# Optimization experiments

Measured on AMD Instinct MI355X. Metric: run time of the kernel, lower is better.

Reference implementation:

```python
import jax, jax.numpy as jnp
import numpy as np

V = 10000  # vocab_size
E = 128    # embedding_dim
H = 256    # per-layer hidden size
B = 32     # batch
S = 512    # seq_len


def setup_inputs() -> dict:
    key = jax.random.key(0)
    ks = jax.random.split(key, 8)
    input_x = jax.random.randint(ks[0], (B, S), 0, V, dtype=jnp.int32)
    input_y = jax.random.randint(ks[1], (B, S), 0, V, dtype=jnp.int32)
    input_lengths = jax.random.randint(ks[2], (B,), 1, S + 1, dtype=jnp.int32)
    emb_W = jax.random.uniform(ks[3], (V, E), minval=-1.0, maxval=1.0, dtype=jnp.float32)
    k0 = jax.random.normal(ks[4], (E + H, 4 * H), dtype=jnp.float32) * 0.05
    b0 = jnp.zeros((4 * H,), jnp.float32)
    k1 = jax.random.normal(ks[5], (H + H, 4 * H), dtype=jnp.float32) * 0.05
    b1 = jnp.zeros((4 * H,), jnp.float32)
    out_W = jax.random.normal(ks[6], (H, V), dtype=jnp.float32) * 0.05
    out_b = jnp.zeros((V,), jnp.float32)
    return dict(input_x=input_x, input_y=input_y, input_lengths=input_lengths,
                emb_W=emb_W, k0=k0, b0=b0, k1=k1, b1=b1, out_W=out_W, out_b=out_b)


def _lstm_layer(xs, lengths, kernel, bias):
    """TF LSTMCell semantics: gate order i,g,f,o; forget_bias=1.0.
    xs: [S,B,D] -> ys: [S,B,H]; dynamic_rnn masking: state frozen and
    output zeroed for t >= lengths."""
    Sd, Bd, _ = xs.shape
    Hd = bias.shape[0] // 4
    f1 = jnp.asarray(1.0, xs.dtype)

    def step(carry, inp):
        h, c = carry
        x, t = inp
        z = jnp.concatenate([x, h], axis=-1) @ kernel + bias  # [B,4H]
        i, g, f, o = jnp.split(z, 4, axis=-1)
        c_new = jax.nn.sigmoid(f + f1) * c + jax.nn.sigmoid(i) * jnp.tanh(g)
        h_new = jax.nn.sigmoid(o) * jnp.tanh(c_new)
        active = (t < lengths)[:, None]
        h2 = jnp.where(active, h_new, h)
        c2 = jnp.where(active, c_new, c)
        out = jnp.where(active, h_new, jnp.zeros_like(h_new))
        return (h2, c2), out

    init = (jnp.zeros((Bd, Hd), xs.dtype), jnp.zeros((Bd, Hd), xs.dtype))
    _, ys = jax.lax.scan(step, init, (xs, jnp.arange(Sd)))
    return ys


def reference(input_x, input_y, input_lengths, emb_W, k0, b0, k1, b1, out_W, out_b):
    emb = emb_W[input_x]                 # [B,S,E] embedding lookup
    xs = jnp.swapaxes(emb, 0, 1)         # [S,B,E]
    h1 = _lstm_layer(xs, input_lengths, k0, b0)
    h2 = _lstm_layer(h1, input_lengths, k1, b1)
    outputs = jnp.swapaxes(h2, 0, 1)     # [B,S,H]
    scores = outputs @ out_W + out_b     # [B,S,V]
    logp = jax.nn.log_softmax(scores, axis=-1)
    xent = -jnp.take_along_axis(logp, input_y[..., None], axis=-1)[..., 0]  # [B,S]
    mask = jnp.sign(input_y.astype(scores.dtype))  # label 0 is padding
    per_ex = jnp.sum(mask * xent, axis=1) / input_lengths.astype(scores.dtype)
    return jnp.mean(per_ex)
```

## Files before the change

kernel.cpp:

```cpp
#include <hip/hip_runtime.h>
#include <hip/hip_fp8.h>
#include <cmath>

#define SS 512
#define BB 32
#define EE 128
#define HH 256
#define VV 10000
#define NROWS (SS*BB)
#define VPAD 10048
#define NT8 (VPAD/16)

typedef unsigned short ushort_t;
typedef unsigned char uchar_t;
typedef __attribute__((ext_vector_type(8))) short bf16x8;
typedef __attribute__((ext_vector_type(8))) int i32x8;
typedef __attribute__((ext_vector_type(4))) float f32x4;

#define MFMA(a,b,c)  __builtin_amdgcn_mfma_f32_16x16x32_bf16((a),(b),(c),0,0,0)
#define MFMAS(a,b,c) __builtin_amdgcn_mfma_scale_f32_16x16x128_f8f6f4((a),(b),(c),0,0,0,0x7F7F7F7F,0,0x7F7F7F7F)

__device__ __forceinline__ ushort_t f2bf(float x) {
    unsigned u = __float_as_uint(x);
    u = (u + 0x7FFFu + ((u >> 16) & 1u)) >> 16;
    return (ushort_t)u;
}
__device__ __forceinline__ float bf2f(ushort_t h) {
    return __uint_as_float(((unsigned)h) << 16);
}
__device__ __forceinline__ uchar_t f2fp8(float x) {
    __hip_fp8_e4m3 t(x);
    return (uchar_t)t.__x;
}
__device__ __forceinline__ float sigf(float x) { return 1.0f / (1.0f + __expf(-x)); }
__device__ __forceinline__ float tanhf_(float x) { return 1.0f - 2.0f / (__expf(2.0f * x) + 1.0f); }

__device__ __forceinline__ i32x8 ldfrag(const uchar_t* base, int lane) {
    i32x8 r;
    ((uint4*)&r)[0] = *(const uint4*)(base + lane * 16);
    ((uint4*)&r)[1] = *(const uint4*)(base + 1024 + lane * 16);
    return r;
}

__device__ __forceinline__ void pollc(unsigned* p, unsigned target) {
    int it = 0;
    while (__hip_atomic_load(p, __ATOMIC_RELAXED, __HIP_MEMORY_SCOPE_AGENT) < target) {
        __builtin_amdgcn_s_sleep(4);
        if (++it > 50000000) break;
    }
}
__device__ __forceinline__ void reladd(unsigned* p) {
    __hip_atomic_fetch_add(p, 1u, __ATOMIC_RELEASE, __HIP_MEMORY_SCOPE_AGENT);
}

__global__ __launch_bounds__(256)
void prep_kernel(const float* __restrict__ k0, const float* __restrict__ k1,
                 const float* __restrict__ out_W, const float* __restrict__ out_b,
                 ushort_t* __restrict__ W1xT, uchar_t* __restrict__ Wsw1,
                 uchar_t* __restrict__ Wsw2, ushort_t* __restrict__ W2x,
                 uchar_t* __restrict__ Wt8, float* __restrict__ obp)
{
    __shared__ float tile[64][65];
    const int blk = blockIdx.x;
    const int tid = threadIdx.x;

    if (blk < 32) {
        const int n0 = (blk & 15) * 64, k0_ = (blk >> 4) * 64;
        for (int i = tid; i < 4096; i += 256) {
            const int kk = i >> 6, nn = i & 63;
            tile[kk][nn] = k0[(size_t)(k0_ + kk) * 1024 + n0 + nn];
        }
        __syncthreads();
        for (int i = tid; i < 4096; i += 256) {
            const int nn = i >> 6, kk = i & 63;
            W1xT[(size_t)(n0 + nn) * 128 + k0_ + kk] = f2bf(tile[kk][nn]);
        }
    } else if (blk < 160) {
        const bool l2 = (blk >= 96);
        const int nt = l2 ? (blk - 96) : (blk - 32);
        const float* src = l2 ? (k1 + (size_t)HH * 1024) : (k0 + (size_t)EE * 1024);
        uchar_t* dst = l2 ? Wsw2 : Wsw1;
        const int kk = tid >> 7, h = (tid >> 6) & 1, l = tid & 63;
        const int q = l >> 4, n16 = l & 15;
        const int col = (nt >> 4) * 256 + (nt & 15) * 16 + n16;
        uchar_t v[16];
#pragma unroll
        for (int j = 0; j < 16; j++) {
            const int k = kk * 128 + q * 32 + h * 16 + j;
            v[j] = f2fp8(src[(size_t)k * 1024 + col]);
        }
        *(uint4*)&dst[(((size_t)(nt * 2 + kk) * 2 + h) * 64 + l) * 16] = *(uint4*)v;
    } else if (blk < 224) {
        const int r = blk - 160;
        const int n0 = (r & 15) * 64, k0_ = (r >> 4) * 64;
        for (int i = tid; i < 4096; i += 256) {
            const int kk = i >> 6, nn = i & 63;
            tile[kk][nn] = k1[(size_t)(k0_ + kk) * 1024 + n0 + nn];
        }
        __syncthreads();
        for (int i = tid; i < 4096; i += 256) {
            const int nn = i >> 6, kk = i & 63;
            W2x[(size_t)(n0 + nn) * 256 + k0_ + kk] = f2bf(tile[kk][nn]);
        }
    } else if (blk < 224 + NT8) {
        const int nt = blk - 224;
        const int kk = tid >> 7, h = (tid >> 6) & 1, l = tid & 63;
        const int q = l >> 4, n16 = l & 15;
        const int col = nt * 16 + n16;
        uchar_t v[16];
#pragma unroll
        for (int j = 0; j < 16; j++) {
            const int k = kk * 128 + q * 32 + h * 16 + j;
            v[j] = (col < VV) ? f2fp8(out_W[(size_t)k * VV + col]) : (uchar_t)0;
        }
        *(uint4*)&Wt8[(((size_t)(nt * 2 + kk) * 2 + h) * 64 + l) * 16] = *(uint4*)v;
    } else {
        const int v = (blk - 224 - NT8) * 256 + tid;
        if (v < VPAD) obp[v] = (v < VV) ? out_b[v] : -INFINITY;
    }
}

__global__ __launch_bounds__(256)
void zgemm_mf(const ushort_t* __restrict__ W1xT, const float* __restrict__ b0v,
              const float* __restrict__ emb, const int* __restrict__ idx,
              ushort_t* __restrict__ Zb)
{
    __shared__ ushort_t ash[64 * 136];
    const int tid = threadIdx.x;
    const int w = tid >> 6, lane = tid & 63;
    const int q = lane >> 4, n16 = lane & 15;
    const int m0 = blockIdx.x * 64;
    const int nbase = blockIdx.y * 256;

    for (int i = tid; i < 64 * 32; i += 256) {
        const int r_ = i >> 5, c4 = i & 31;
        const int m = m0 + r_;
        const int t = m >> 5, b = m & 31;
        const int id = idx[b * SS + t];
        const float4 v = ((const float4*)emb)[(size_t)id * 32 + c4];
        ushort_t o4[4] = { f2bf(v.x), f2bf(v.y), f2bf(v.z), f2bf(v.w) };
        *(uint2*)&ash[r_ * 136 + c4 * 4] = *(uint2*)o4;
    }
    __syncthreads();

    bf16x8 A[4];
#pragma unroll
    for (int kb = 0; kb < 4; kb++)
        A[kb] = *(const bf16x8*)&ash[(w * 16 + n16) * 136 + kb * 32 + q * 8];

#pragma unroll 1
    for (int nt = 0; nt < 16; nt++) {
        const int n = nbase + nt * 16 + n16;
        bf16x8 B[4];
#pragma unroll
        for (int kb = 0; kb < 4; kb++)
            B[kb] = *(const bf16x8*)&W1xT[(size_t)n * 128 + kb * 32 + q * 8];
        f32x4 C = (f32x4){0.f, 0.f, 0.f, 0.f};
#pragma unroll
        for (int kb = 0; kb < 4; kb++)
            C = MFMA(A[kb], B[kb], C);
        const float bv = b0v[n];
        const int g = n >> 8, u = n & 255;
#pragma unroll
        for (int r = 0; r < 4; r++)
            Zb[(size_t)(m0 + w * 16 + q * 4 + r) * 1024 + u * 4 + g] = f2bf(C[r] + bv);
    }
}

__device__ __forceinline__ void lstm_role(
    uchar_t* Bl, uchar_t* h8buf,
    const uchar_t* __restrict__ Wsw, const ushort_t* __restrict__ zin,
    const int* __restrict__ lens, ushort_t* __restrict__ outp,
    uchar_t* __restrict__ hf8,
    unsigned* prog1, unsigned* xflag, unsigned* h2prog,
    int b, bool isL1)
{
    uchar_t (*h8)[256] = (uchar_t (*)[256])h8buf;
    const int tid = threadIdx.x;
    const int w = tid >> 6, lane = tid & 63;
    const int q = lane >> 4, n16 = lane & 15;
    const int len = lens[b];
    const int jown = q >> 1;
    const int unit = w * 32 + jown * 16 + n16;

#pragma unroll
    for (int li = 0; li < 3; li++) {
        const int nt = li * 16 + w * 2 + 1;
#pragma unroll
        for (int fh = 0; fh < 4; fh++) {
            const size_t s = (((size_t)nt * 4 + fh) * 64 + lane) * 16;
            const size_t d = (((size_t)(w * 3 + li) * 4 + fh) * 64 + lane) * 16;
            *(uint4*)&Bl[d] = *(const uint4*)&Wsw[s];
        }
    }
    i32x8 Bv[4][2];
#pragma unroll
    for (int g = 0; g < 4; g++) {
        const int nt = g * 16 + w * 2;
#pragma unroll
        for (int kk = 0; kk < 2; kk++)
            Bv[g][kk] = ldfrag(&Wsw[(size_t)nt * 4096 + kk * 2048], lane);
    }
    i32x8 Sv[2];
    {
        const int nt = 3 * 16 + w * 2 + 1;
#pragma unroll
        for (int kk = 0; kk < 2; kk++)
            Sv[kk] = ldfrag(&Wsw[(size_t)nt * 4096 + kk * 2048], lane);
    }
    if (tid < 256) { h8[0][tid] = 0; h8[1][tid] = 0; }
    float c = 0.f;
    __syncthreads();

    const uchar_t* Lb0 = &Bl[(size_t)(w * 3) * 4096];

    uint2 zreg;
    bool zvalid = false;
    if (isL1) {
        zreg = *(const uint2*)&zin[(size_t)(0 * 32 + b) * 1024 + unit * 4];
        zvalid = true;
    }

    for (int t = 0; t < SS; t++) {
        if (t >= len) {
            uint4 zz; zz.x = zz.y = zz.z = zz.w = 0u;
            if (outp) {
                const int nseg = (SS - t) * 32;
                for (int i = tid; i < nseg; i += 512) {
                    const int tt = t + (i >> 5), seg = i & 31;
                    *(uint4*)&outp[((size_t)tt * 32 + b) * 256 + seg * 8] = zz;
                }
            }
            if (hf8) {
                const int nseg8 = (SS - t) * 16;
                for (int i = tid; i < nseg8; i += 512) {
                    const int tt = t + (i >> 4), seg = i & 15;
                    *(uint4*)&hf8[((size_t)tt * 32 + b) * 256 + seg * 16] = zz;
                }
            }
            __syncthreads();
            if (tid == 0) {
                if (isL1) for (int cc = t >> 5; cc < 16; cc++) reladd(&prog1[cc]);
                else      for (int cc = t >> 3; cc < 64; cc++) reladd(&h2prog[cc]);
            }
            break;
        }
        if (!isL1 && (t & 31) == 0) {
            if (tid == 0) {
#pragma unroll
                for (int cc = 0; cc < 4; cc++) pollc(&xflag[(t >> 3) + cc], 1u);
            }
            __syncthreads();
            __builtin_amdgcn_fence(__ATOMIC_ACQUIRE, "agent");
        }
        const size_t row = (size_t)t * 32 + b;
        ushort_t z4[4];
        if (zvalid) *(uint2*)z4 = zreg;
        else        *(uint2*)z4 = *(const uint2*)&zin[row * 1024 + unit * 4];
        if (t + 1 < SS && (isL1 || ((t + 1) & 31) != 0)) {
            zreg = *(const uint2*)&zin[(row + 32) * 1024 + unit * 4];
            zvalid = true;
        } else zvalid = false;

        const int rd = t & 1, wr = rd ^ 1;
        i32x8 Af0, Af1;
        ((uint4*)&Af0)[0] = *(const uint4*)&h8[rd][q * 32];
        ((uint4*)&Af0)[1] = *(const uint4*)&h8[rd][q * 32 + 16];
        ((uint4*)&Af1)[0] = *(const uint4*)&h8[rd][128 + q * 32];
        ((uint4*)&Af1)[1] = *(const uint4*)&h8[rd][128 + q * 32 + 16];

        float gvv[4];
#pragma unroll
        for (int g = 0; g < 4; g++) {
            f32x4 C0 = (f32x4){0.f,0.f,0.f,0.f}, C1 = (f32x4){0.f,0.f,0.f,0.f};
            C0 = MFMAS(Af0, Bv[g][0], C0);
            C0 = MFMAS(Af1, Bv[g][1], C0);
            if (g < 3) {
                const uchar_t* p = Lb0 + (size_t)g * 4096;
                C1 = MFMAS(Af0, ldfrag(p, lane), C1);
                C1 = MFMAS(Af1, ldfrag(p + 2048, lane), C1);
            } else {
                C1 = MFMAS(Af0, Sv[0], C1);
                C1 = MFMAS(Af1, Sv[1], C1);
            }
            gvv[g] = jown ? C1[0] : C0[0];
        }
        {
            const float zi = bf2f(z4[0]) + gvv[0];
            const float zg = bf2f(z4[1]) + gvv[1];
            const float zf = bf2f(z4[2]) + gvv[2];
            const float zo = bf2f(z4[3]) + gvv[3];
            const float cn = sigf(zf + 1.0f) * c + sigf(zi) * tanhf_(zg);
            const float hn = sigf(zo) * tanhf_(cn);
            c = cn;
            const uchar_t h8v = f2fp8(hn);
            h8[wr][unit] = h8v;
            if (outp) outp[row * 256 + unit] = f2bf(hn);
            if (hf8) hf8[row * 256 + unit] = h8v;
        }
        __syncthreads();
        if (tid == 0) {
            if (isL1) { if (((t + 1) & 31) == 0) reladd(&prog1[t >> 5]); }
            else      { if (((t + 1) & 7)  == 0) reladd(&h2prog[t >> 3]); }
        }
    }
}

__global__ __launch_bounds__(512, 1)
void pipe_kernel(const uchar_t* __restrict__ Wsw1, const uchar_t* __restrict__ Wsw2,
                 const ushort_t* __restrict__ W2x, const float* __restrict__ b1v,
                 const int* __restrict__ lens, const ushort_t* __restrict__ Zb,
                 ushort_t* __restrict__ out1, ushort_t* __restrict__ Xp,
                 uchar_t* __restrict__ hf8, const uchar_t* __restrict__ Wt8,
                 const float* __restrict__ obp, const int* __restrict__ y,
                 float* __restrict__ out,
                 unsigned* __restrict__ prog1, unsigned* __restrict__ xflag,
                 unsigned* __restrict__ h2prog)
{
    __shared__ uchar_t smem[98816];
    const int tid = threadIdx.x;
    const int blk = blockIdx.x;
    const int w = tid >> 6, lane = tid & 63;
    const int q = lane >> 4, n16 = lane & 15;

    if (blk < 32) {
        lstm_role(smem, smem + 98304, Wsw1, Zb, lens, out1, nullptr,
                  prog1, xflag, h2prog, blk, true);
    } else if (blk < 96) {
        ushort_t* ash = (ushort_t*)smem;
        const int b2 = blk - 32;
        if (tid == 0) pollc(&prog1[b2 >> 2], 32u);
        __syncthreads();
        __builtin_amdgcn_fence(__ATOMIC_ACQUIRE, "agent");
#pragma unroll 1
        for (int half = 0; half < 2; half++) {
            const int m0 = b2 * 256 + half * 128;
            if (half) __syncthreads();
            for (int i = tid; i < 128 * 32; i += 512) {
                const int r_ = i >> 5, s_ = i & 31;
                *(uint4*)&ash[r_ * 264 + s_ * 8] =
                    *(const uint4*)&out1[(size_t)(m0 + r_) * 256 + s_ * 8];
            }
            __syncthreads();
#pragma unroll 1
            for (int i = 0; i < 8; i++) {
                const int n = (w * 8 + i) * 16 + n16;
                bf16x8 Bfr[8];
#pragma unroll
                for (int kb = 0; kb < 8; kb++)
                    Bfr[kb] = *(const bf16x8*)&W2x[(size_t)n * 256 + kb * 32 + q * 8];
                const float bval = b1v[n];
                const int g = n >> 8, u = n & 255;
                f32x4 Cc[8];
#pragma unroll
                for (int mt = 0; mt < 8; mt++) {
                    Cc[mt] = (f32x4){0.f, 0.f, 0.f, 0.f};
                    bf16x8 Af[8];
#pragma unroll
                    for (int kb = 0; kb < 8; kb++)
                        Af[kb] = *(const bf16x8*)&ash[(mt * 16 + n16) * 264 + kb * 32 + q * 8];
#pragma unroll
                    for (int kb = 0; kb < 8; kb++)
                        Cc[mt] = MFMA(Af[kb], Bfr[kb], Cc[mt]);
                }
#pragma unroll
                for (int mt = 0; mt < 8; mt++)
#pragma unroll
                    for (int r = 0; r < 4; r++) {
                        const int rrow = m0 + mt * 16 + q * 4 + r;
                        Xp[(size_t)rrow * 1024 + u * 4 + g] = f2bf(Cc[mt][r] + bval);
                    }
            }
        }
        __syncthreads();
        if (tid == 0)
            __hip_atomic_store(&xflag[b2], 1u, __ATOMIC_RELEASE, __HIP_MEMORY_SCOPE_AGENT);
    } else if (blk < 128) {
        lstm_role(smem, smem + 98304, Wsw2, Xp, lens, nullptr, hf8,
                  prog1, xflag, h2prog, blk - 96, false);
    } else {
        float* lsw = (float*)smem;
        float* tgt64 = (float*)(smem + 1024);
        const int cb = blk - 128;
        if (tid == 0) pollc(&h2prog[cb >> 1], 32u);
        __syncthreads();
        __builtin_amdgcn_fence(__ATOMIC_ACQUIRE, "agent");
#pragma unroll 1
        for (int half = 0; half < 2; half++) {
            const int m0 = cb * 128 + half * 64;
            __syncthreads();
            if (tid < 64) tgt64[tid] = 0.f;
            i32x8 A8[4][2];
            int yv[16];
            float lsum[16];
            if (tid < 256) {
#pragma unroll
                for (int mt = 0; mt < 4; mt++) {
                    const size_t rbase = (size_t)(m0 + mt * 16 + n16) * 256;
#pragma unroll
                    for (int kk = 0; kk < 2; kk++) {
                        ((uint4*)&A8[mt][kk])[0] = *(const uint4*)&hf8[rbase + kk * 128 + q * 32];
                        ((uint4*)&A8[mt][kk])[1] = *(const uint4*)&hf8[rbase + kk * 128 + q * 32 + 16];
                    }
                }
#pragma unroll
                for (int mt = 0; mt < 4; mt++)
#pragma unroll
                    for (int r = 0; r < 4; r++) {
                        const int m = m0 + mt * 16 + q * 4 + r;
                        yv[mt * 4 + r] = y[(m & 31) * SS + (m >> 5)];
                    }
#pragma unroll
                for (int i = 0; i < 16; i++) lsum[i] = 0.f;
            }
            __syncthreads();
            if (tid < 256) {
                for (int tile = 0; tile < 157; tile++) {
                    const int nt = w * 157 + tile;
                    const int n = nt * 16 + n16;
                    const i32x8 B0 = ldfrag(&Wt8[(size_t)(nt * 2 + 0) * 2048], lane);
                    const i32x8 B1 = ldfrag(&Wt8[(size_t)(nt * 2 + 1) * 2048], lane);
                    const float obv = obp[n];
                    f32x4 C[4];
#pragma unroll
                    for (int mt = 0; mt < 4; mt++) {
                        C[mt] = (f32x4){0.f, 0.f, 0.f, 0.f};
                        C[mt] = MFMAS(A8[mt][0], B0, C[mt]);
                        C[mt] = MFMAS(A8[mt][1], B1, C[mt]);
                    }
#pragma unroll
                    for (int mt = 0; mt < 4; mt++)
#pragma unroll
                        for (int r = 0; r < 4; r++) {
                            const float sc = C[mt][r] + obv;
                            if (n == yv[mt * 4 + r]) tgt64[mt * 16 + q * 4 + r] = sc;
                            lsum[mt * 4 + r] += __expf(sc - 16.0f);
                        }
                }
#pragma unroll
                for (int i = 0; i < 16; i++) {
                    float v = lsum[i];
                    v += __shfl_xor(v, 1, 16); v += __shfl_xor(v, 2, 16);
                    v += __shfl_xor(v, 4, 16); v += __shfl_xor(v, 8, 16);
                    lsum[i] = v;
                }
                if (n16 == 0)
#pragma unroll
                    for (int i = 0; i < 16; i++)
                        lsw[w * 64 + (i >> 2) * 16 + q * 4 + (i & 3)] = lsum[i];
            }
            __syncthreads();
            if (tid < 64) {
                const float l = lsw[tid] + lsw[64 + tid] + lsw[128 + tid] + lsw[192 + tid];
                const float lse = 16.0f + __logf(l);
                const int m = m0 + tid;
                const int tt = m >> 5, bb = m & 31;
                const int yvv = y[bb * SS + tt];
                float local = (yvv != 0) ? (lse - tgt64[tid]) / (32.0f * (float)lens[bb]) : 0.f;
                for (int off = 1; off < 64; off <<= 1) local += __shfl_xor(local, off, 64);
                if (tid == 0) atomicAdd(out, local);
            }
        }
    }
}

extern "C" void kernel_launch(void* const* d_in, const int* in_sizes, int n_in,
                              void* d_out, int out_size, void* d_ws, size_t ws_size,
                              hipStream_t stream)
{
    const int*   input_x = (const int*)  d_in[0];
    const int*   input_y = (const int*)  d_in[1];
    const int*   lens    = (const int*)  d_in[2];
    const float* emb_W   = (const float*)d_in[3];
    const float* k0      = (const float*)d_in[4];
    const float* b0      = (const float*)d_in[5];
    const float* k1      = (const float*)d_in[6];
    const float* b1      = (const float*)d_in[7];
    const float* out_W   = (const float*)d_in[8];
    const float* out_b   = (const float*)d_in[9];
    float* out = (float*)d_out;

    char* p = (char*)d_ws;
    ushort_t* Zb   = (ushort_t*)p;  p += (size_t)NROWS * 1024 * 2;
    ushort_t* Xp   = (ushort_t*)p;  p += (size_t)NROWS * 1024 * 2;
    ushort_t* out1 = (ushort_t*)p;  p += (size_t)NROWS * 256 * 2;
    uchar_t*  h2f8 = (uchar_t*)p;   p += (size_t)NROWS * 256;
    uchar_t*  Wsw1 = (uchar_t*)p;   p += (size_t)1024 * 256;
    uchar_t*  Wsw2 = (uchar_t*)p;   p += (size_t)1024 * 256;
    ushort_t* W2x  = (ushort_t*)p;  p += (size_t)1024 * 256 * 2;
    ushort_t* W1xT = (ushort_t*)p;  p += (size_t)1024 * 128 * 2;
    uchar_t*  Wt8  = (uchar_t*)p;   p += (size_t)NT8 * 4096;
    float*    obp  = (float*)p;     p += (size_t)VPAD * 4;
    unsigned* prog1  = (unsigned*)p; p += 16 * 4;
    unsigned* xflag  = (unsigned*)p; p += 64 * 4;
    unsigned* h2prog = (unsigned*)p; p += 64 * 4;

    hipMemsetAsync(d_out, 0, sizeof(float), stream);
    hipMemsetAsync(prog1, 0, 144 * 4, stream);

    prep_kernel<<<224 + NT8 + 40, 256, 0, stream>>>(k0, k1, out_W, out_b,
                                                    W1xT, Wsw1, Wsw2, W2x, Wt8, obp);
    zgemm_mf<<<dim3(256, 4), 256, 0, stream>>>(W1xT, b0, emb_W, input_x, Zb);
    pipe_kernel<<<256, 512, 0, stream>>>(Wsw1, Wsw2, W2x, b1, lens, Zb, out1, Xp,
                                         h2f8, Wt8, obp, input_y, out,
                                         prog1, xflag, h2prog);
}
```

Measured before the change: 1.155 ms.

## Fuse layer-1 input GEMM into persistent pipeline kernel with progress flags

Removes the separate zgemm launch and has the 128 idle scoring blocks of the persistent pipeline kernel compute the embedding-times-W1x pre-activations first, publishing per-chunk progress counters. Layer-1 LSTM blocks now poll a zprog counter every 32 timesteps before reading Zb, so the recurrence can begin before the whole input GEMM finishes. This removes a kernel boundary and overlaps the GEMM with the recurrent start, at the cost of extra polling and synchronization in the layer-1 loop.

```diff
diff --git a/kernel.cpp b/kernel.cpp
--- a/kernel.cpp
+++ b/kernel.cpp
@@ -120,59 +120,12 @@
     }
 }
 
-__global__ __launch_bounds__(256)
-void zgemm_mf(const ushort_t* __restrict__ W1xT, const float* __restrict__ b0v,
-              const float* __restrict__ emb, const int* __restrict__ idx,
-              ushort_t* __restrict__ Zb)
-{
-    __shared__ ushort_t ash[64 * 136];
-    const int tid = threadIdx.x;
-    const int w = tid >> 6, lane = tid & 63;
-    const int q = lane >> 4, n16 = lane & 15;
-    const int m0 = blockIdx.x * 64;
-    const int nbase = blockIdx.y * 256;
-
-    for (int i = tid; i < 64 * 32; i += 256) {
-        const int r_ = i >> 5, c4 = i & 31;
-        const int m = m0 + r_;
-        const int t = m >> 5, b = m & 31;
-        const int id = idx[b * SS + t];
-        const float4 v = ((const float4*)emb)[(size_t)id * 32 + c4];
-        ushort_t o4[4] = { f2bf(v.x), f2bf(v.y), f2bf(v.z), f2bf(v.w) };
-        *(uint2*)&ash[r_ * 136 + c4 * 4] = *(uint2*)o4;
-    }
-    __syncthreads();
-
-    bf16x8 A[4];
-#pragma unroll
-    for (int kb = 0; kb < 4; kb++)
-        A[kb] = *(const bf16x8*)&ash[(w * 16 + n16) * 136 + kb * 32 + q * 8];
-
-#pragma unroll 1
-    for (int nt = 0; nt < 16; nt++) {
-        const int n = nbase + nt * 16 + n16;
-        bf16x8 B[4];
-#pragma unroll
-        for (int kb = 0; kb < 4; kb++)
-            B[kb] = *(const bf16x8*)&W1xT[(size_t)n * 128 + kb * 32 + q * 8];
-        f32x4 C = (f32x4){0.f, 0.f, 0.f, 0.f};
-#pragma unroll
-        for (int kb = 0; kb < 4; kb++)
-            C = MFMA(A[kb], B[kb], C);
-        const float bv = b0v[n];
-        const int g = n >> 8, u = n & 255;
-#pragma unroll
-        for (int r = 0; r < 4; r++)
-            Zb[(size_t)(m0 + w * 16 + q * 4 + r) * 1024 + u * 4 + g] = f2bf(C[r] + bv);
-    }
-}
-
 __device__ __forceinline__ void lstm_role(
     uchar_t* Bl, uchar_t* h8buf,
     const uchar_t* __restrict__ Wsw, const ushort_t* __restrict__ zin,
     const int* __restrict__ lens, ushort_t* __restrict__ outp,
     uchar_t* __restrict__ hf8,
-    unsigned* prog1, unsigned* xflag, unsigned* h2prog,
+    unsigned* prog1, unsigned* xflag, unsigned* h2prog, unsigned* zprog,
     int b, bool isL1)
 {
     uchar_t (*h8)[256] = (uchar_t (*)[256])h8buf;
@@ -216,10 +169,6 @@
 
     uint2 zreg;
     bool zvalid = false;
-    if (isL1) {
-        zreg = *(const uint2*)&zin[(size_t)(0 * 32 + b) * 1024 + unit * 4];
-        zvalid = true;
-    }
 
     for (int t = 0; t < SS; t++) {
         if (t >= len) {
@@ -245,10 +194,13 @@
             }
             break;
         }
-        if (!isL1 && (t & 31) == 0) {
+        if ((t & 31) == 0) {
             if (tid == 0) {
-#pragma unroll
-                for (int cc = 0; cc < 4; cc++) pollc(&xflag[(t >> 3) + cc], 1u);
+                if (isL1) pollc(&zprog[t >> 5], 8u);
+                else {
+#pragma unroll
+                    for (int cc = 0; cc < 4; cc++) pollc(&xflag[(t >> 3) + cc], 1u);
+                }
             }
             __syncthreads();
             __builtin_amdgcn_fence(__ATOMIC_ACQUIRE, "agent");
@@ -257,7 +209,7 @@
         ushort_t z4[4];
         if (zvalid) *(uint2*)z4 = zreg;
         else        *(uint2*)z4 = *(const uint2*)&zin[row * 1024 + unit * 4];
-        if (t + 1 < SS && (isL1 || ((t + 1) & 31) != 0)) {
+        if (t + 1 < SS && ((t + 1) & 31) != 0) {
             zreg = *(const uint2*)&zin[(row + 32) * 1024 + unit * 4];
             zvalid = true;
         } else zvalid = false;
@@ -309,13 +261,15 @@
 __global__ __launch_bounds__(512, 1)
 void pipe_kernel(const uchar_t* __restrict__ Wsw1, const uchar_t* __restrict__ Wsw2,
                  const ushort_t* __restrict__ W2x, const float* __restrict__ b1v,
-                 const int* __restrict__ lens, const ushort_t* __restrict__ Zb,
+                 const int* __restrict__ lens, ushort_t* __restrict__ Zb,
                  ushort_t* __restrict__ out1, ushort_t* __restrict__ Xp,
                  uchar_t* __restrict__ hf8, const uchar_t* __restrict__ Wt8,
                  const float* __restrict__ obp, const int* __restrict__ y,
                  float* __restrict__ out,
+                 const ushort_t* __restrict__ W1xT, const float* __restrict__ b0v,
+                 const float* __restrict__ emb, const int* __restrict__ idx,
                  unsigned* __restrict__ prog1, unsigned* __restrict__ xflag,
-                 unsigned* __restrict__ h2prog)
+                 unsigned* __restrict__ h2prog, unsigned* __restrict__ zprog)
 {
     __shared__ uchar_t smem[98816];
     const int tid = threadIdx.x;
@@ -325,7 +279,7 @@
 
     if (blk < 32) {
         lstm_role(smem, smem + 98304, Wsw1, Zb, lens, out1, nullptr,
-                  prog1, xflag, h2prog, blk, true);
+                  prog1, xflag, h2prog, zprog, blk, true);
     } else if (blk < 96) {
         ushort_t* ash = (ushort_t*)smem;
         const int b2 = blk - 32;
@@ -377,11 +331,55 @@
             __hip_atomic_store(&xflag[b2], 1u, __ATOMIC_RELEASE, __HIP_MEMORY_SCOPE_AGENT);
     } else if (blk < 128) {
         lstm_role(smem, smem + 98304, Wsw2, Xp, lens, nullptr, hf8,
-                  prog1, xflag, h2prog, blk - 96, false);
+                  prog1, xflag, h2prog, zprog, blk - 96, false);
     } else {
+        const int cb = blk - 128;
+        {
+            ushort_t* ash = (ushort_t*)smem;
+#pragma unroll 1
+            for (int u8 = 0; u8 < 8; u8++) {
+                const int mb = cb * 2 + (u8 >> 2);
+                const int nbase = (u8 & 3) * 256;
+                const int m0 = mb * 64;
+                if (u8) __syncthreads();
+                for (int i = tid; i < 64 * 32; i += 512) {
+                    const int r_ = i >> 5, c4 = i & 31;
+                    const int m = m0 + r_;
+                    const int t = m >> 5, b = m & 31;
+                    const int id = idx[b * SS + t];
+                    const float4 v = ((const float4*)emb)[(size_t)id * 32 + c4];
+                    ushort_t o4[4] = { f2bf(v.x), f2bf(v.y), f2bf(v.z), f2bf(v.w) };
+                    *(uint2*)&ash[r_ * 136 + c4 * 4] = *(uint2*)o4;
+                }
+                __syncthreads();
+                const int mt = w & 3, nh = w >> 2;
+                bf16x8 A[4];
+#pragma unroll
+                for (int kb = 0; kb < 4; kb++)
+                    A[kb] = *(const bf16x8*)&ash[(mt * 16 + n16) * 136 + kb * 32 + q * 8];
+#pragma unroll 1
+                for (int nt = nh * 8; nt < nh * 8 + 8; nt++) {
+                    const int n = nbase + nt * 16 + n16;
+                    bf16x8 B[4];
+#pragma unroll
+                    for (int kb = 0; kb < 4; kb++)
+                        B[kb] = *(const bf16x8*)&W1xT[(size_t)n * 128 + kb * 32 + q * 8];
+                    f32x4 C = (f32x4){0.f, 0.f, 0.f, 0.f};
+#pragma unroll
+                    for (int kb = 0; kb < 4; kb++)
+                        C = MFMA(A[kb], B[kb], C);
+                    const float bv = b0v[n];
+                    const int g = n >> 8, u = n & 255;
+#pragma unroll
+                    for (int r = 0; r < 4; r++)
+                        Zb[(size_t)(m0 + mt * 16 + q * 4 + r) * 1024 + u * 4 + g] = f2bf(C[r] + bv);
+                }
+            }
+            __syncthreads();
+            if (tid == 0) reladd(&zprog[cb >> 3]);
+        }
         float* lsw = (float*)smem;
         float* tgt64 = (float*)(smem + 1024);
-        const int cb = blk - 128;
         if (tid == 0) pollc(&h2prog[cb >> 1], 32u);
         __syncthreads();
         __builtin_amdgcn_fence(__ATOMIC_ACQUIRE, "agent");
@@ -447,7 +445,7 @@
                 if (n16 == 0)
 #pragma unroll
                     for (int i = 0; i < 16; i++)
-                        lsw[w * 64 + (i >> 2) * 16 + q * 4 + (i & 3)] = lsum[i];
+                        lsw[(w & 3) * 64 + (i >> 2) * 16 + q * 4 + (i & 3)] = lsum[i];
             }
             __syncthreads();
             if (tid < 64) {
@@ -494,14 +492,15 @@
     unsigned* prog1  = (unsigned*)p; p += 16 * 4;
     unsigned* xflag  = (unsigned*)p; p += 64 * 4;
     unsigned* h2prog = (unsigned*)p; p += 64 * 4;
+    unsigned* zprog  = (unsigned*)p; p += 16 * 4;
 
     hipMemsetAsync(d_out, 0, sizeof(float), stream);
-    hipMemsetAsync(prog1, 0, 144 * 4, stream);
+    hipMemsetAsync(prog1, 0, 160 * 4, stream);
 
     prep_kernel<<<224 + NT8 + 40, 256, 0, stream>>>(k0, k1, out_W, out_b,
                                                     W1xT, Wsw1, Wsw2, W2x, Wt8, obp);
-    zgemm_mf<<<dim3(256, 4), 256, 0, stream>>>(W1xT, b0, emb_W, input_x, Zb);
     pipe_kernel<<<256, 512, 0, stream>>>(Wsw1, Wsw2, W2x, b1, lens, Zb, out1, Xp,
                                          h2f8, Wt8, obp, input_y, out,
-                                         prog1, xflag, h2prog);
-}
+                                         W1xT, b0, emb_W, input_x,
+                                         prog1, xflag, h2prog, zprog);
+}
```

Result: slower. 1.206 ms (+4.4%).
